# Optimization experiments

Measured on AMD Instinct MI355X. Metric: run time of the kernel, lower is better.

Reference implementation:

```python
import jax, jax.numpy as jnp
import numpy as np

N_HEADS = 16
CHUNK = 128  # chunk size for blocked causal linear attention


def _phi(x):
    # feature map: elu(x) + 1 (strictly positive)
    return jax.nn.elu(x) + 1.0


def setup_inputs() -> dict:
    key = jax.random.key(0)
    ks = jax.random.split(key, 5)
    d = 1024
    scale = (2.0 / (d + d)) ** 0.5  # xavier_uniform-like std
    W = lambda k: jax.random.normal(k, (d, d), jnp.float32) * scale
    return {
        "x": jax.random.normal(ks[0], (4, 4096, d), jnp.float32),
        "Wq": W(ks[1]), "bq": jnp.zeros((d,), jnp.float32),
        "Wk": W(ks[2]), "bk": jnp.zeros((d,), jnp.float32),
        "Wv": W(ks[3]), "bv": jnp.zeros((d,), jnp.float32),
        "Wo": W(ks[4]), "bo": jnp.zeros((d,), jnp.float32),
    }


def reference(x, Wq, bq, Wk, bk, Wv, bv, Wo, bo):
    b, s, dm = x.shape
    h = N_HEADS
    d = dm // h

    def proj(W, bias):
        # (b, s, dm) -> (b*h, s, d)
        y = x @ W.T + bias
        return y.reshape(b, s, h, d).transpose(0, 2, 1, 3).reshape(b * h, s, d)

    q = _phi(proj(Wq, bq))
    k = _phi(proj(Wk, bk))
    v = proj(Wv, bv)

    C = CHUNK
    n = s // C
    # (b*h, s, d) -> (n_chunks, b*h, C, d) for scan over chunks
    to_chunks = lambda t: t.reshape(b * h, n, C, d).transpose(1, 0, 2, 3)
    qc, kc, vc = to_chunks(q), to_chunks(k), to_chunks(v)
    mask = jnp.tril(jnp.ones((C, C), bool))  # causal within chunk

    def step(carry, inp):
        S, z = carry  # S: (bh, d, d) running sum of k v^T; z: (bh, d) running sum of k
        qi, ki, vi = inp  # each (bh, C, d)
        scores = jnp.einsum('bqd,bkd->bqk', qi, ki)
        scores = jnp.where(mask, scores, jnp.zeros((), scores.dtype))
        num = jnp.einsum('bqk,bkd->bqd', scores, vi) + jnp.einsum('bqd,bde->bqe', qi, S)
        kcum = jnp.cumsum(ki, axis=1) + z[:, None, :]
        den = jnp.sum(qi * kcum, axis=-1, keepdims=True)
        out = num / den
        S2 = S + jnp.einsum('bkd,bke->bde', ki, vi)
        z2 = z + ki.sum(axis=1)
        return (S2, z2), out

    init = (jnp.zeros((b * h, d, d), x.dtype), jnp.zeros((b * h, d), x.dtype))
    _, outs = jax.lax.scan(step, init, (qc, kc, vc))  # outs: (n, bh, C, d)
    out = outs.transpose(1, 0, 2, 3).reshape(b, h, s, d).transpose(0, 2, 1, 3).reshape(b, s, dm)
    return out @ Wo.T + bo
```

## Files before the change

kernel.cpp:

```cpp
#include <hip/hip_runtime.h>
#include <hip/hip_bf16.h>

typedef __attribute__((ext_vector_type(8))) short bf16x8;
typedef __attribute__((ext_vector_type(4))) short bf16x4;
typedef __attribute__((ext_vector_type(4))) float floatx4;
typedef unsigned short u16;
typedef unsigned int u32;

#define DM 1024
#define SEQ 4096
#define NH 16
#define HD 64
#define CHUNK 128

__device__ __forceinline__ float bf2f(u16 x) {
    u32 u = ((u32)x) << 16;
    return __builtin_bit_cast(float, u);
}
__device__ __forceinline__ u16 f2bf(float f) {
    u32 u = __builtin_bit_cast(u32, f);
    u32 r = u + 0x7FFF + ((u >> 16) & 1);
    return (u16)(r >> 16);
}
__device__ __forceinline__ bf16x8 cvt8(const float* p) {
    floatx4 a = *(const floatx4*)p;
    floatx4 b = *(const floatx4*)(p + 4);
    bf16x8 r;
    r[0] = (short)f2bf(a[0]); r[1] = (short)f2bf(a[1]);
    r[2] = (short)f2bf(a[2]); r[3] = (short)f2bf(a[3]);
    r[4] = (short)f2bf(b[0]); r[5] = (short)f2bf(b[1]);
    r[6] = (short)f2bf(b[2]); r[7] = (short)f2bf(b[3]);
    return r;
}
__device__ __forceinline__ void async_copy16(const u16* gsrc, u16* ldst) {
    __builtin_amdgcn_global_load_lds(
        (const __attribute__((address_space(1))) void*)gsrc,
        (__attribute__((address_space(3))) void*)ldst, 16, 0, 0);
}

__global__ void cvt_w_k(const float* __restrict__ Wq, const float* __restrict__ Wk,
                        const float* __restrict__ Wv, const float* __restrict__ Wo,
                        u16* __restrict__ Wqkv, u16* __restrict__ Wob)
{
    int g = blockIdx.x * 256 + threadIdx.x;
    int w = g >> 17;
    int off = g & 131071;
    const float* src = (w == 0) ? Wq : (w == 1) ? Wk : (w == 2) ? Wv : Wo;
    u16* dst = (w < 3) ? (Wqkv + ((size_t)w << 20)) : Wob;
    *(bf16x8*)&dst[(size_t)off * 8] = cvt8(src + (size_t)off * 8);
}

__global__ void cvt_x_k(const float* __restrict__ xs, u16* __restrict__ xb)
{
    size_t g = (size_t)blockIdx.x * 256 + threadIdx.x;
    *(bf16x8*)&xb[g * 8] = cvt8(xs + g * 8);
}

__global__ __launch_bounds__(256, 2) void qkv_gemm_k(
    const u16* __restrict__ xb, const u16* __restrict__ Wqkv,
    const float* __restrict__ bq, const float* __restrict__ bk,
    const float* __restrict__ bv,
    u16* __restrict__ Qh, u16* __restrict__ Kh, u16* __restrict__ Vh)
{
    __shared__ __align__(16) u16 aSh[128 * 64];
    __shared__ __align__(16) u16 bSh[128 * 64];
    int t = threadIdx.x, lane = t & 63, w = t >> 6;
    int q = lane >> 4, ln = lane & 15;
    int wm = (w & 1) * 64, wn = (w >> 1) * 64;
    int n0 = blockIdx.x * 128, m0 = blockIdx.y * 128;
    int wgr = t & 192;
    floatx4 acc[4][4] = {};

    for (int k0 = 0; k0 < DM; k0 += 64) {
#pragma unroll
        for (int i = 0; i < 4; ++i) {
            int gi = i * 256 + t;
            int r = gi >> 3;
            int c = (gi & 7) ^ (r & 7);
            async_copy16(xb + (size_t)(m0 + r) * DM + k0 + c * 8,
                         aSh + (size_t)(i * 256 + wgr) * 8);
            async_copy16(Wqkv + (size_t)(n0 + r) * DM + k0 + c * 8,
                         bSh + (size_t)(i * 256 + wgr) * 8);
        }
        __builtin_amdgcn_s_waitcnt(0);
        __syncthreads();
#pragma unroll
        for (int ks = 0; ks < 2; ++ks) {
            int cg = ks * 4 + q;
            bf16x8 af[4], bfv[4];
#pragma unroll
            for (int tm = 0; tm < 4; ++tm) {
                int m = wm + tm * 16 + ln;
                af[tm] = *(const bf16x8*)&aSh[(m * 8 + (cg ^ (m & 7))) * 8];
            }
#pragma unroll
            for (int tn = 0; tn < 4; ++tn) {
                int n = wn + tn * 16 + ln;
                bfv[tn] = *(const bf16x8*)&bSh[(n * 8 + (cg ^ (n & 7))) * 8];
            }
#pragma unroll
            for (int tm = 0; tm < 4; ++tm)
#pragma unroll
                for (int tn = 0; tn < 4; ++tn)
                    acc[tm][tn] = __builtin_amdgcn_mfma_f32_16x16x32_bf16(
                        af[tm], bfv[tn], acc[tm][tn], 0, 0, 0);
        }
        __syncthreads();
    }
#pragma unroll
    for (int tn = 0; tn < 4; ++tn) {
        int gn = n0 + wn + tn * 16 + ln;
        int proj = gn >> 10, col = gn & 1023;
        float bb = ((proj == 0) ? bq : (proj == 1) ? bk : bv)[col];
        u16* plane = (proj == 0) ? Qh : (proj == 1) ? Kh : Vh;
        int head = col >> 6, dl = col & 63;
#pragma unroll
        for (int tm = 0; tm < 4; ++tm) {
            int gmb = m0 + wm + tm * 16 + q * 4;
#pragma unroll
            for (int r = 0; r < 4; ++r) {
                int gm = gmb + r;
                float v = acc[tm][tn][r] + bb;
                if (proj < 2) v = (v > 0.f) ? (v + 1.f) : __expf(v);
                plane[(((size_t)(gm >> 12) * NH + head) * SEQ + (gm & 4095)) * HD + dl]
                    = f2bf(v);
            }
        }
    }
}

__global__ __launch_bounds__(256, 2) void out_gemm_k(
    const u16* __restrict__ Ah, const u16* __restrict__ Wob,
    const float* __restrict__ bo, float* __restrict__ out)
{
    __shared__ __align__(16) u16 aSh[128 * 64];
    __shared__ __align__(16) u16 bSh[128 * 64];
    int t = threadIdx.x, lane = t & 63, w = t >> 6;
    int q = lane >> 4, ln = lane & 15;
    int wm = (w & 1) * 64, wn = (w >> 1) * 64;
    int n0 = blockIdx.x * 128, m0 = blockIdx.y * 128;
    int wgr = t & 192;
    floatx4 acc[4][4] = {};

    for (int k0 = 0; k0 < DM; k0 += 64) {
#pragma unroll
        for (int i = 0; i < 4; ++i) {
            int gi = i * 256 + t;
            int r = gi >> 3;
            int c = (gi & 7) ^ (r & 7);
            int rr = m0 + r;
            async_copy16(Ah + (((size_t)((rr >> 12) * NH + (k0 >> 6))) << 18)
                            + (size_t)((rr & 4095) << 6) + (size_t)(c * 8),
                         aSh + (size_t)(i * 256 + wgr) * 8);
            async_copy16(Wob + (size_t)(n0 + r) * DM + k0 + c * 8,
                         bSh + (size_t)(i * 256 + wgr) * 8);
        }
        __builtin_amdgcn_s_waitcnt(0);
        __syncthreads();
#pragma unroll
        for (int ks = 0; ks < 2; ++ks) {
            int cg = ks * 4 + q;
            bf16x8 af[4], bfv[4];
#pragma unroll
            for (int tm = 0; tm < 4; ++tm) {
                int m = wm + tm * 16 + ln;
                af[tm] = *(const bf16x8*)&aSh[(m * 8 + (cg ^ (m & 7))) * 8];
            }
#pragma unroll
            for (int tn = 0; tn < 4; ++tn) {
                int n = wn + tn * 16 + ln;
                bfv[tn] = *(const bf16x8*)&bSh[(n * 8 + (cg ^ (n & 7))) * 8];
            }
#pragma unroll
            for (int tm = 0; tm < 4; ++tm)
#pragma unroll
                for (int tn = 0; tn < 4; ++tn)
                    acc[tm][tn] = __builtin_amdgcn_mfma_f32_16x16x32_bf16(
                        af[tm], bfv[tn], acc[tm][tn], 0, 0, 0);
        }
        __syncthreads();
    }
#pragma unroll
    for (int tn = 0; tn < 4; ++tn) {
        int gn = n0 + wn + tn * 16 + ln;
        float bb = bo[gn];
#pragma unroll
        for (int tm = 0; tm < 4; ++tm) {
            int gmb = m0 + wm + tm * 16 + q * 4;
#pragma unroll
            for (int r = 0; r < 4; ++r)
                out[(size_t)(gmb + r) * DM + gn] = acc[tm][tn][r] + bb;
        }
    }
}

__global__ __launch_bounds__(256, 1) void chunk_stats_k(
    const u16* __restrict__ Kh, const u16* __restrict__ Vh,
    u16* __restrict__ Sc, float* __restrict__ Zc)
{
    __shared__ __align__(16) u16 kSh[128 * 64];
    __shared__ __align__(16) u16 vSh[128 * 64];
    __shared__ float zpart[4][64];
    int t = threadIdx.x;
    int bhc = blockIdx.x;
    const u16* Kb = Kh + ((size_t)(bhc >> 5) * SEQ + (size_t)(bhc & 31) * CHUNK) * HD;
    const u16* Vb = Vh + ((size_t)(bhc >> 5) * SEQ + (size_t)(bhc & 31) * CHUNK) * HD;
#pragma unroll
    for (int i = 0; i < 4; ++i) {
        int g = i * 256 + t;
        *(bf16x8*)&kSh[g * 8] = *(const bf16x8*)&Kb[(size_t)g * 8];
        *(bf16x8*)&vSh[g * 8] = *(const bf16x8*)&Vb[(size_t)g * 8];
    }
    __syncthreads();
    int tD = t & 15, tE = t >> 4;
    float acc[4][4] = {};
#pragma unroll 8
    for (int r = 0; r < 128; ++r) {
        bf16x4 vq = *(const bf16x4*)&vSh[r * 64 + tE * 4];
        bf16x4 kq = *(const bf16x4*)&kSh[r * 64 + tD * 4];
        float vf[4], kf[4];
#pragma unroll
        for (int i = 0; i < 4; ++i) { vf[i] = bf2f((u16)vq[i]); kf[i] = bf2f((u16)kq[i]); }
#pragma unroll
        for (int a = 0; a < 4; ++a)
#pragma unroll
            for (int b = 0; b < 4; ++b) acc[a][b] += vf[a] * kf[b];
    }
    u16* So = Sc + (size_t)bhc * HD * HD;
#pragma unroll
    for (int a = 0; a < 4; ++a) {
        bf16x4 sv;
#pragma unroll
        for (int b = 0; b < 4; ++b) sv[b] = (short)f2bf(acc[a][b]);
        *(bf16x4*)&So[(tE * 4 + a) * HD + tD * 4] = sv;
    }
    {
        int dz = t & 63, qz = t >> 6;
        float z = 0.f;
#pragma unroll
        for (int r = 0; r < 32; ++r) z += bf2f(kSh[(qz * 32 + r) * 64 + dz]);
        zpart[qz][dz] = z;
    }
    __syncthreads();
    if (t < 64)
        Zc[(size_t)bhc * HD + t] =
            zpart[0][t] + zpart[1][t] + zpart[2][t] + zpart[3][t];
}

__global__ void prefix_k(u16* __restrict__ Sc, float* __restrict__ Zc)
{
    int bh = blockIdx.x, y = blockIdx.y, t = threadIdx.x;
    if (y < 32) {
        size_t base = (size_t)bh * 32 * 4096 + y * 128 + t;
        u16 vals[32];
#pragma unroll
        for (int c = 0; c < 32; ++c) vals[c] = Sc[base + (size_t)c * 4096];
        float run = 0.f;
#pragma unroll
        for (int c = 0; c < 32; ++c) {
            float cur = bf2f(vals[c]);
            Sc[base + (size_t)c * 4096] = f2bf(run);
            run += cur;
        }
    } else if (t < 64) {
        size_t base = (size_t)bh * 32 * 64 + t;
        float zv[32];
#pragma unroll
        for (int c = 0; c < 32; ++c) zv[c] = Zc[base + (size_t)c * 64];
        float run = 0.f;
#pragma unroll
        for (int c = 0; c < 32; ++c) {
            Zc[base + (size_t)c * 64] = run;
            run += zv[c];
        }
    }
}

__global__ __launch_bounds__(256, 1) void attn_out_k(
    const u16* Qh, const u16* __restrict__ Kh,
    const u16* __restrict__ Vh, const u16* __restrict__ Sp,
    const float* __restrict__ Zp, u16* Qw)
{
    __shared__ __align__(16) u16 vtSh[64 * 136];
    __shared__ __align__(16) u16 pSh[128 * 136];
    __shared__ float psum[128];
    __shared__ float qzs[128];
    int t = threadIdx.x, lane = t & 63, w = t >> 6;
    int q = lane >> 4, ln = lane & 15;
    int bhc = blockIdx.x, bh = bhc >> 5, ch = bhc & 31;
    const u16* Qb = Qh + ((size_t)bh * SEQ + (size_t)ch * CHUNK) * HD;
    const u16* Kb = Kh + ((size_t)bh * SEQ + (size_t)ch * CHUNK) * HD;
    const u16* Vb = Vh + ((size_t)bh * SEQ + (size_t)ch * CHUNK) * HD;
    const u16* Spb = Sp + (size_t)bhc * HD * HD;
    const float* Zpb = Zp + (size_t)bhc * HD;

#pragma unroll
    for (int i = 0; i < 4; ++i) {
        int g = i * 256 + t;
        int k = g >> 3, e0 = (g & 7) * 8;
        bf16x8 vv = *(const bf16x8*)&Vb[(size_t)k * HD + e0];
#pragma unroll
        for (int j = 0; j < 8; ++j) vtSh[(e0 + j) * 136 + k] = (u16)vv[j];
    }

    int wm = (w & 1) * 64, wn = (w >> 1) * 64;
    bf16x8 afr[2][4];
#pragma unroll
    for (int ks = 0; ks < 2; ++ks)
#pragma unroll
        for (int tm = 0; tm < 4; ++tm) {
            int m = wm + tm * 16 + ln;
            afr[ks][tm] = *(const bf16x8*)&Qb[(size_t)m * HD + ks * 32 + q * 8];
        }
    floatx4 acc[4][4] = {};
#pragma unroll
    for (int ks = 0; ks < 2; ++ks) {
        bf16x8 bfr[4];
#pragma unroll
        for (int tn = 0; tn < 4; ++tn) {
            int n = wn + tn * 16 + ln;
            bfr[tn] = *(const bf16x8*)&Kb[(size_t)n * HD + ks * 32 + q * 8];
        }
#pragma unroll
        for (int tm = 0; tm < 4; ++tm)
#pragma unroll
            for (int tn = 0; tn < 4; ++tn)
                acc[tm][tn] = __builtin_amdgcn_mfma_f32_16x16x32_bf16(
                    afr[ks][tm], bfr[tn], acc[tm][tn], 0, 0, 0);
    }
#pragma unroll
    for (int tm = 0; tm < 4; ++tm) {
        int rb = wm + tm * 16 + q * 4;
#pragma unroll
        for (int tn = 0; tn < 4; ++tn) {
            int cc = wn + tn * 16 + ln;
#pragma unroll
            for (int r = 0; r < 4; ++r) {
                float v = (cc <= rb + r) ? acc[tm][tn][r] : 0.f;
                pSh[(rb + r) * 136 + cc] = f2bf(v);
            }
        }
    }
    __syncthreads();
    if (t < 128) {
        const u16* prow = &pSh[t * 136];
        float s = 0.f;
#pragma unroll
        for (int i = 0; i < 16; ++i) {
            bf16x8 pv = *(const bf16x8*)&prow[i * 8];
#pragma unroll
            for (int j = 0; j < 8; ++j) s += bf2f((u16)pv[j]);
        }
        psum[t] = s;
    } else {
        int row = t - 128;
        float s = 0.f;
#pragma unroll
        for (int i = 0; i < 8; ++i) {
            bf16x8 qv = *(const bf16x8*)&Qb[(size_t)row * HD + i * 8];
#pragma unroll
            for (int j = 0; j < 8; ++j) s += bf2f((u16)qv[j]) * Zpb[i * 8 + j];
        }
        qzs[row] = s;
    }
    __syncthreads();

    int wn2 = (w >> 1) * 32;
    floatx4 acc2[4][2] = {};
#pragma unroll
    for (int ks = 0; ks < 4; ++ks) {
        bf16x8 ap[4], bv[2];
#pragma unroll
        for (int tm = 0; tm < 4; ++tm) {
            int m = wm + tm * 16 + ln;
            ap[tm] = *(const bf16x8*)&pSh[m * 136 + ks * 32 + q * 8];
        }
#pragma unroll
        for (int tn = 0; tn < 2; ++tn) {
            int n = wn2 + tn * 16 + ln;
            bv[tn] = *(const bf16x8*)&vtSh[n * 136 + ks * 32 + q * 8];
        }
#pragma unroll
        for (int tm = 0; tm < 4; ++tm)
#pragma unroll
            for (int tn = 0; tn < 2; ++tn)
                acc2[tm][tn] = __builtin_amdgcn_mfma_f32_16x16x32_bf16(
                    ap[tm], bv[tn], acc2[tm][tn], 0, 0, 0);
    }
#pragma unroll
    for (int ks = 0; ks < 2; ++ks) {
        bf16x8 bs[2];
#pragma unroll
        for (int tn = 0; tn < 2; ++tn) {
            int n = wn2 + tn * 16 + ln;
            bs[tn] = *(const bf16x8*)&Spb[(size_t)n * HD + ks * 32 + q * 8];
        }
#pragma unroll
        for (int tm = 0; tm < 4; ++tm)
#pragma unroll
            for (int tn = 0; tn < 2; ++tn)
                acc2[tm][tn] = __builtin_amdgcn_mfma_f32_16x16x32_bf16(
                    afr[ks][tm], bs[tn], acc2[tm][tn], 0, 0, 0);
    }
    __syncthreads();
#pragma unroll
    for (int tm = 0; tm < 4; ++tm) {
        int rb = wm + tm * 16 + q * 4;
#pragma unroll
        for (int r = 0; r < 4; ++r) {
            int mrow = rb + r;
            float inv = 1.0f / fmaxf(psum[mrow] + qzs[mrow], 1e-20f);
#pragma unroll
            for (int tn = 0; tn < 2; ++tn) {
                int e = wn2 + tn * 16 + ln;
                pSh[mrow * 72 + e] = f2bf(acc2[tm][tn][r] * inv);
            }
        }
    }
    __syncthreads();
    size_t obase = ((size_t)bh * SEQ + (size_t)ch * CHUNK) * HD;
#pragma unroll
    for (int j = 0; j < 4; ++j) {
        int ci = j * 256 + t;
        *(bf16x8*)&Qw[obase + (size_t)ci * 8] =
            *(const bf16x8*)&pSh[(ci >> 3) * 72 + (ci & 7) * 8];
    }
}

extern "C" void kernel_launch(void* const* d_in, const int* in_sizes, int n_in,
                              void* d_out, int out_size, void* d_ws, size_t ws_size,
                              hipStream_t stream) {
    const float* x  = (const float*)d_in[0];
    const float* Wq = (const float*)d_in[1];
    const float* bq = (const float*)d_in[2];
    const float* Wk = (const float*)d_in[3];
    const float* bk = (const float*)d_in[4];
    const float* Wv = (const float*)d_in[5];
    const float* bv = (const float*)d_in[6];
    const float* Wo = (const float*)d_in[7];
    const float* bo = (const float*)d_in[8];
    float* out = (float*)d_out;

    const size_t PLANE = (size_t)NH * SEQ * HD;
    const size_t FIXED = (3 * (size_t)DM * DM + (size_t)DM * DM) * 2;
    const size_t PER_BATCH = 4 * PLANE * 2 + (size_t)NH * 32 * 4096 * 2
                           + (size_t)NH * 32 * HD * 4;
    if (ws_size < FIXED + PER_BATCH) return;
    int nb = (ws_size >= FIXED + 4 * PER_BATCH) ? 4
           : (ws_size >= FIXED + 2 * PER_BATCH) ? 2 : 1;

    char* p0 = (char*)d_ws;
    u16* Wqkv = (u16*)p0;                       p0 += 3 * (size_t)DM * DM * 2;
    u16* Wob  = (u16*)p0;                       p0 += (size_t)DM * DM * 2;

    cvt_w_k<<<dim3(2048), dim3(256), 0, stream>>>(Wq, Wk, Wv, Wo, Wqkv, Wob);

    for (int b0 = 0; b0 < 4; b0 += nb) {
        char* p = p0;
        u16* xb = (u16*)p;  p += (size_t)nb * PLANE * 2;
        u16* Qh = (u16*)p;  p += (size_t)nb * PLANE * 2;
        u16* Kh = (u16*)p;  p += (size_t)nb * PLANE * 2;
        u16* Vh = (u16*)p;  p += (size_t)nb * PLANE * 2;
        u16* Sc = (u16*)p;  p += (size_t)nb * NH * 32 * 4096 * 2;
        float* Zc = (float*)p;
        const float* xs = x + (size_t)b0 * SEQ * DM;

        cvt_x_k<<<dim3(nb * 2048), dim3(256), 0, stream>>>(xs, xb);
        qkv_gemm_k<<<dim3(24, nb * 32), dim3(256), 0, stream>>>(
            xb, Wqkv, bq, bk, bv, Qh, Kh, Vh);
        chunk_stats_k<<<dim3(nb * 512), dim3(256), 0, stream>>>(Kh, Vh, Sc, Zc);
        prefix_k<<<dim3(nb * 16, 33), dim3(128), 0, stream>>>(Sc, Zc);
        attn_out_k<<<dim3(nb * 512), dim3(256), 0, stream>>>(Qh, Kh, Vh, Sc, Zc, Qh);
        out_gemm_k<<<dim3(8, nb * 32), dim3(256), 0, stream>>>(
            Qh, Wob, bo, out + (size_t)b0 * SEQ * DM);
    }
}
```

Baseline: 381.4 us.

## Rewrite projection GEMMs as 256x256 double-buffered pipelined kernels with swizzled tiles

```diff
diff --git a/kernel.cpp b/kernel.cpp
--- a/kernel.cpp
+++ b/kernel.cpp
@@ -56,71 +56,138 @@
     *(bf16x8*)&xb[g * 8] = cvt8(xs + g * 8);
 }
 
-__global__ __launch_bounds__(256, 2) void qkv_gemm_k(
+template<int CS>
+__device__ __forceinline__ void stage_half(const u16* src, int ld, u16* ldsM,
+                                           int h, int t) {
+#pragma unroll
+    for (int j = 0; j < 2; ++j) {
+        int r  = j * 64 + (t >> 3);
+        int c  = (t & 7) ^ (r & 7);
+        int gr = ((r / CS) * 2 + h) * CS + (r % CS);
+        int wr = j * 64 + ((t & 448) >> 3);
+        int gw = ((wr / CS) * 2 + h) * CS + (wr % CS);
+        async_copy16(src + (size_t)gr * ld + (size_t)c * 8,
+                     ldsM + (size_t)gw * 64);
+    }
+}
+
+__device__ __forceinline__ void ld_a_quad(const u16* aB, int mbase, int ln, int q,
+                                          bf16x8 (&af)[4][2]) {
+#pragma unroll
+    for (int fm = 0; fm < 4; ++fm)
+#pragma unroll
+        for (int ks = 0; ks < 2; ++ks) {
+            int m = mbase + fm * 16 + ln, cg = ks * 4 + q;
+            af[fm][ks] = *(const bf16x8*)&aB[(m * 8 + (cg ^ (m & 7))) * 8];
+        }
+}
+__device__ __forceinline__ void ld_b_pair(const u16* bB, int nbase, int ln, int q,
+                                          bf16x8 (&bf)[2][2]) {
+#pragma unroll
+    for (int fn = 0; fn < 2; ++fn)
+#pragma unroll
+        for (int ks = 0; ks < 2; ++ks) {
+            int n = nbase + fn * 16 + ln, cg = ks * 4 + q;
+            bf[fn][ks] = *(const bf16x8*)&bB[(n * 8 + (cg ^ (n & 7))) * 8];
+        }
+}
+__device__ __forceinline__ void mfma16(const bf16x8 (&af)[4][2],
+                                       const bf16x8 (&bf)[2][2],
+                                       floatx4 (&acc)[8][4], int hm, int gn) {
+#pragma unroll
+    for (int ks = 0; ks < 2; ++ks)
+#pragma unroll
+        for (int fm = 0; fm < 4; ++fm)
+#pragma unroll
+            for (int fn = 0; fn < 2; ++fn)
+                acc[hm * 4 + fm][gn * 2 + fn] =
+                    __builtin_amdgcn_mfma_f32_16x16x32_bf16(
+                        af[fm][ks], bf[fn][ks], acc[hm * 4 + fm][gn * 2 + fn],
+                        0, 0, 0);
+}
+
+#define PH_MID() do { __builtin_amdgcn_sched_barrier(0);                      \
+    __builtin_amdgcn_s_barrier();                                             \
+    asm volatile("s_waitcnt lgkmcnt(0)" ::: "memory");                        \
+    __builtin_amdgcn_sched_barrier(0);                                        \
+    __builtin_amdgcn_s_setprio(1); } while (0)
+#define PH_END() do { __builtin_amdgcn_s_setprio(0);                          \
+    __builtin_amdgcn_sched_barrier(0);                                        \
+    __builtin_amdgcn_s_barrier(); } while (0)
+
+__global__ __launch_bounds__(512, 2) void qkv_gemm_k(
     const u16* __restrict__ xb, const u16* __restrict__ Wqkv,
     const float* __restrict__ bq, const float* __restrict__ bk,
     const float* __restrict__ bv,
     u16* __restrict__ Qh, u16* __restrict__ Kh, u16* __restrict__ Vh)
 {
-    __shared__ __align__(16) u16 aSh[128 * 64];
-    __shared__ __align__(16) u16 bSh[128 * 64];
-    int t = threadIdx.x, lane = t & 63, w = t >> 6;
+    __shared__ __align__(16) u16 lds[2][32768];
+    int t = threadIdx.x, lane = t & 63;
     int q = lane >> 4, ln = lane & 15;
-    int wm = (w & 1) * 64, wn = (w >> 1) * 64;
-    int n0 = blockIdx.x * 128, m0 = blockIdx.y * 128;
-    int wgr = t & 192;
-    floatx4 acc[4][4] = {};
-
-    for (int k0 = 0; k0 < DM; k0 += 64) {
-#pragma unroll
-        for (int i = 0; i < 4; ++i) {
-            int gi = i * 256 + t;
-            int r = gi >> 3;
-            int c = (gi & 7) ^ (r & 7);
-            async_copy16(xb + (size_t)(m0 + r) * DM + k0 + c * 8,
-                         aSh + (size_t)(i * 256 + wgr) * 8);
-            async_copy16(Wqkv + (size_t)(n0 + r) * DM + k0 + c * 8,
-                         bSh + (size_t)(i * 256 + wgr) * 8);
-        }
-        __builtin_amdgcn_s_waitcnt(0);
-        __syncthreads();
-#pragma unroll
-        for (int ks = 0; ks < 2; ++ks) {
-            int cg = ks * 4 + q;
-            bf16x8 af[4], bfv[4];
-#pragma unroll
-            for (int tm = 0; tm < 4; ++tm) {
-                int m = wm + tm * 16 + ln;
-                af[tm] = *(const bf16x8*)&aSh[(m * 8 + (cg ^ (m & 7))) * 8];
-            }
-#pragma unroll
-            for (int tn = 0; tn < 4; ++tn) {
-                int n = wn + tn * 16 + ln;
-                bfv[tn] = *(const bf16x8*)&bSh[(n * 8 + (cg ^ (n & 7))) * 8];
-            }
-#pragma unroll
-            for (int tm = 0; tm < 4; ++tm)
-#pragma unroll
-                for (int tn = 0; tn < 4; ++tn)
-                    acc[tm][tn] = __builtin_amdgcn_mfma_f32_16x16x32_bf16(
-                        af[tm], bfv[tn], acc[tm][tn], 0, 0, 0);
-        }
-        __syncthreads();
-    }
-#pragma unroll
-    for (int tn = 0; tn < 4; ++tn) {
-        int gn = n0 + wn + tn * 16 + ln;
+    int wid = t >> 6;
+    int wmb = (wid >> 2) * 128, wnb = (wid & 3) * 64;
+    int nwg = gridDim.x;
+    int b0i = blockIdx.x;
+    int swz = (b0i & 7) * (nwg >> 3) + (b0i >> 3);
+    int m0 = (swz / 12) * 256, n0 = (swz % 12) * 256;
+
+    const u16* Abase = xb + (size_t)m0 * DM;
+    const u16* Bbase = Wqkv + (size_t)n0 * DM;
+    floatx4 acc[8][4] = {};
+
+    stage_half<64>(Abase + 0,  DM, &lds[0][0],     0, t);
+    stage_half<32>(Bbase + 0,  DM, &lds[0][16384], 1, t);
+    stage_half<64>(Abase + 0,  DM, &lds[0][0],     1, t);
+    stage_half<32>(Bbase + 0,  DM, &lds[0][16384], 0, t);
+    stage_half<64>(Abase + 64, DM, &lds[1][0],     0, t);
+    stage_half<32>(Bbase + 64, DM, &lds[1][16384], 1, t);
+    asm volatile("s_waitcnt vmcnt(4)" ::: "memory");
+    __builtin_amdgcn_sched_barrier(0);
+    __builtin_amdgcn_s_barrier();
+
+#pragma unroll 2
+    for (int tt = 0; tt < 16; ++tt) {
+        const u16* aB = &lds[tt & 1][0];
+        const u16* bB = &lds[tt & 1][16384];
+        u16* aN = &lds[(tt + 1) & 1][0];
+        u16* bN = &lds[(tt + 1) & 1][16384];
+        u16* aC = &lds[tt & 1][0];
+        u16* bC = &lds[tt & 1][16384];
+        bf16x8 af[4][2], bf0[2][2], bf1[2][2];
+        ld_a_quad(aB, wmb, ln, q, af);
+        ld_b_pair(bB, wnb, ln, q, bf0);
+        if (tt < 15) stage_half<64>(Abase + (tt + 1) * 64, DM, aN, 1, t);
+        PH_MID(); mfma16(af, bf0, acc, 0, 0); PH_END();
+        ld_b_pair(bB, wnb + 32, ln, q, bf1);
+        if (tt < 15) stage_half<32>(Bbase + (tt + 1) * 64, DM, bN, 0, t);
+        PH_MID(); mfma16(af, bf1, acc, 0, 1); PH_END();
+        ld_a_quad(aB, wmb + 64, ln, q, af);
+        if (tt < 14) stage_half<64>(Abase + (tt + 2) * 64, DM, aC, 0, t);
+        PH_MID(); mfma16(af, bf1, acc, 1, 1); PH_END();
+        ld_b_pair(bB, wnb, ln, q, bf0);
+        if (tt < 14) stage_half<32>(Bbase + (tt + 2) * 64, DM, bC, 1, t);
+        PH_MID(); mfma16(af, bf0, acc, 1, 0);
+        __builtin_amdgcn_s_setprio(0);
+        if (tt < 14)       asm volatile("s_waitcnt vmcnt(4)" ::: "memory");
+        else if (tt == 14) asm volatile("s_waitcnt vmcnt(0)" ::: "memory");
+        __builtin_amdgcn_sched_barrier(0);
+        __builtin_amdgcn_s_barrier();
+    }
+
+#pragma unroll
+    for (int fn = 0; fn < 4; ++fn) {
+        int gn = n0 + wnb + fn * 16 + ln;
         int proj = gn >> 10, col = gn & 1023;
         float bb = ((proj == 0) ? bq : (proj == 1) ? bk : bv)[col];
         u16* plane = (proj == 0) ? Qh : (proj == 1) ? Kh : Vh;
         int head = col >> 6, dl = col & 63;
 #pragma unroll
-        for (int tm = 0; tm < 4; ++tm) {
-            int gmb = m0 + wm + tm * 16 + q * 4;
+        for (int fm = 0; fm < 8; ++fm) {
+            int gmb = m0 + wmb + fm * 16 + q * 4;
 #pragma unroll
             for (int r = 0; r < 4; ++r) {
                 int gm = gmb + r;
-                float v = acc[tm][tn][r] + bb;
+                float v = acc[fm][fn][r] + bb;
                 if (proj < 2) v = (v > 0.f) ? (v + 1.f) : __expf(v);
                 plane[(((size_t)(gm >> 12) * NH + head) * SEQ + (gm & 4095)) * HD + dl]
                     = f2bf(v);
@@ -129,67 +196,76 @@
     }
 }
 
-__global__ __launch_bounds__(256, 2) void out_gemm_k(
+__global__ __launch_bounds__(512, 2) void out_gemm_k(
     const u16* __restrict__ Ah, const u16* __restrict__ Wob,
     const float* __restrict__ bo, float* __restrict__ out)
 {
-    __shared__ __align__(16) u16 aSh[128 * 64];
-    __shared__ __align__(16) u16 bSh[128 * 64];
-    int t = threadIdx.x, lane = t & 63, w = t >> 6;
+    __shared__ __align__(16) u16 lds[2][32768];
+    int t = threadIdx.x, lane = t & 63;
     int q = lane >> 4, ln = lane & 15;
-    int wm = (w & 1) * 64, wn = (w >> 1) * 64;
-    int n0 = blockIdx.x * 128, m0 = blockIdx.y * 128;
-    int wgr = t & 192;
-    floatx4 acc[4][4] = {};
-
-    for (int k0 = 0; k0 < DM; k0 += 64) {
-#pragma unroll
-        for (int i = 0; i < 4; ++i) {
-            int gi = i * 256 + t;
-            int r = gi >> 3;
-            int c = (gi & 7) ^ (r & 7);
-            int rr = m0 + r;
-            async_copy16(Ah + (((size_t)((rr >> 12) * NH + (k0 >> 6))) << 18)
-                            + (size_t)((rr & 4095) << 6) + (size_t)(c * 8),
-                         aSh + (size_t)(i * 256 + wgr) * 8);
-            async_copy16(Wob + (size_t)(n0 + r) * DM + k0 + c * 8,
-                         bSh + (size_t)(i * 256 + wgr) * 8);
-        }
-        __builtin_amdgcn_s_waitcnt(0);
-        __syncthreads();
-#pragma unroll
-        for (int ks = 0; ks < 2; ++ks) {
-            int cg = ks * 4 + q;
-            bf16x8 af[4], bfv[4];
-#pragma unroll
-            for (int tm = 0; tm < 4; ++tm) {
-                int m = wm + tm * 16 + ln;
-                af[tm] = *(const bf16x8*)&aSh[(m * 8 + (cg ^ (m & 7))) * 8];
-            }
-#pragma unroll
-            for (int tn = 0; tn < 4; ++tn) {
-                int n = wn + tn * 16 + ln;
-                bfv[tn] = *(const bf16x8*)&bSh[(n * 8 + (cg ^ (n & 7))) * 8];
-            }
-#pragma unroll
-            for (int tm = 0; tm < 4; ++tm)
-#pragma unroll
-                for (int tn = 0; tn < 4; ++tn)
-                    acc[tm][tn] = __builtin_amdgcn_mfma_f32_16x16x32_bf16(
-                        af[tm], bfv[tn], acc[tm][tn], 0, 0, 0);
-        }
-        __syncthreads();
-    }
-#pragma unroll
-    for (int tn = 0; tn < 4; ++tn) {
-        int gn = n0 + wn + tn * 16 + ln;
+    int wid = t >> 6;
+    int wmb = (wid >> 2) * 128, wnb = (wid & 3) * 64;
+    int nwg = gridDim.x;
+    int b0i = blockIdx.x;
+    int swz = (b0i & 7) * (nwg >> 3) + (b0i >> 3);
+    int m0 = (swz / 4) * 256, n0 = (swz % 4) * 256;
+
+    const u16* Bbase = Wob + (size_t)n0 * DM;
+    size_t aBlk = (size_t)(m0 >> 12) * NH;
+    size_t aRow = (size_t)(m0 & 4095) * 64;
+    #define ASRC(tt) (Ah + (aBlk + (tt)) * 262144 + aRow)
+    floatx4 acc[8][4] = {};
+
+    stage_half<64>(ASRC(0), 64, &lds[0][0],     0, t);
+    stage_half<32>(Bbase + 0, DM, &lds[0][16384], 1, t);
+    stage_half<64>(ASRC(0), 64, &lds[0][0],     1, t);
+    stage_half<32>(Bbase + 0, DM, &lds[0][16384], 0, t);
+    stage_half<64>(ASRC(1), 64, &lds[1][0],     0, t);
+    stage_half<32>(Bbase + 64, DM, &lds[1][16384], 1, t);
+    asm volatile("s_waitcnt vmcnt(4)" ::: "memory");
+    __builtin_amdgcn_sched_barrier(0);
+    __builtin_amdgcn_s_barrier();
+
+#pragma unroll 2
+    for (int tt = 0; tt < 16; ++tt) {
+        const u16* aB = &lds[tt & 1][0];
+        const u16* bB = &lds[tt & 1][16384];
+        u16* aN = &lds[(tt + 1) & 1][0];
+        u16* bN = &lds[(tt + 1) & 1][16384];
+        u16* aC = &lds[tt & 1][0];
+        u16* bC = &lds[tt & 1][16384];
+        bf16x8 af[4][2], bf0[2][2], bf1[2][2];
+        ld_a_quad(aB, wmb, ln, q, af);
+        ld_b_pair(bB, wnb, ln, q, bf0);
+        if (tt < 15) stage_half<64>(ASRC(tt + 1), 64, aN, 1, t);
+        PH_MID(); mfma16(af, bf0, acc, 0, 0); PH_END();
+        ld_b_pair(bB, wnb + 32, ln, q, bf1);
+        if (tt < 15) stage_half<32>(Bbase + (tt + 1) * 64, DM, bN, 0, t);
+        PH_MID(); mfma16(af, bf1, acc, 0, 1); PH_END();
+        ld_a_quad(aB, wmb + 64, ln, q, af);
+        if (tt < 14) stage_half<64>(ASRC(tt + 2), 64, aC, 0, t);
+        PH_MID(); mfma16(af, bf1, acc, 1, 1); PH_END();
+        ld_b_pair(bB, wnb, ln, q, bf0);
+        if (tt < 14) stage_half<32>(Bbase + (tt + 2) * 64, DM, bC, 1, t);
+        PH_MID(); mfma16(af, bf0, acc, 1, 0);
+        __builtin_amdgcn_s_setprio(0);
+        if (tt < 14)       asm volatile("s_waitcnt vmcnt(4)" ::: "memory");
+        else if (tt == 14) asm volatile("s_waitcnt vmcnt(0)" ::: "memory");
+        __builtin_amdgcn_sched_barrier(0);
+        __builtin_amdgcn_s_barrier();
+    }
+    #undef ASRC
+
+#pragma unroll
+    for (int fn = 0; fn < 4; ++fn) {
+        int gn = n0 + wnb + fn * 16 + ln;
         float bb = bo[gn];
 #pragma unroll
-        for (int tm = 0; tm < 4; ++tm) {
-            int gmb = m0 + wm + tm * 16 + q * 4;
+        for (int fm = 0; fm < 8; ++fm) {
+            int gmb = m0 + wmb + fm * 16 + q * 4;
 #pragma unroll
             for (int r = 0; r < 4; ++r)
-                out[(size_t)(gmb + r) * DM + gn] = acc[tm][tn][r] + bb;
+                out[(size_t)(gmb + r) * DM + gn] = acc[fm][fn][r] + bb;
         }
     }
 }
@@ -466,12 +542,12 @@
         const float* xs = x + (size_t)b0 * SEQ * DM;
 
         cvt_x_k<<<dim3(nb * 2048), dim3(256), 0, stream>>>(xs, xb);
-        qkv_gemm_k<<<dim3(24, nb * 32), dim3(256), 0, stream>>>(
+        qkv_gemm_k<<<dim3(12 * nb * 16), dim3(512), 0, stream>>>(
             xb, Wqkv, bq, bk, bv, Qh, Kh, Vh);
         chunk_stats_k<<<dim3(nb * 512), dim3(256), 0, stream>>>(Kh, Vh, Sc, Zc);
         prefix_k<<<dim3(nb * 16, 33), dim3(128), 0, stream>>>(Sc, Zc);
         attn_out_k<<<dim3(nb * 512), dim3(256), 0, stream>>>(Qh, Kh, Vh, Sc, Zc, Qh);
-        out_gemm_k<<<dim3(8, nb * 32), dim3(256), 0, stream>>>(
+        out_gemm_k<<<dim3(4 * nb * 16), dim3(512), 0, stream>>>(
             Qh, Wob, bo, out + (size_t)b0 * SEQ * DM);
     }
 }
```

Result: slower. 404.9 us (+6.2%).

## Stage QKV epilogue through LDS and remap GEMM blocks per XCD

Applied to the files above, without the earlier changes.

```diff
diff --git a/kernel.cpp b/kernel.cpp
--- a/kernel.cpp
+++ b/kernel.cpp
@@ -60,14 +60,20 @@
     const u16* __restrict__ xb, const u16* __restrict__ Wqkv,
     const float* __restrict__ bq, const float* __restrict__ bk,
     const float* __restrict__ bv,
-    u16* __restrict__ Qh, u16* __restrict__ Kh, u16* __restrict__ Vh)
-{
-    __shared__ __align__(16) u16 aSh[128 * 64];
-    __shared__ __align__(16) u16 bSh[128 * 64];
+    u16* __restrict__ Qh, u16* __restrict__ Kh, u16* __restrict__ Vh,
+    int mblocks)
+{
+    __shared__ __align__(16) u16 sh[2][128 * 64];
+    u16* aSh = sh[0];
+    u16* bSh = sh[1];
     int t = threadIdx.x, lane = t & 63, w = t >> 6;
     int q = lane >> 4, ln = lane & 15;
     int wm = (w & 1) * 64, wn = (w >> 1) * 64;
-    int n0 = blockIdx.x * 128, m0 = blockIdx.y * 128;
+    int bid = blockIdx.x;
+    int xcd = bid & 7, local = bid >> 3;
+    int mPerX = mblocks >> 3;
+    int ml = local % mPerX, nn = local / mPerX;
+    int m0 = (xcd * mPerX + ml) * 128, n0 = nn * 128;
     int wgr = t & 192;
     floatx4 acc[4][4] = {};
 
@@ -107,38 +113,58 @@
         }
         __syncthreads();
     }
+    int proj = n0 >> 10, colb = n0 & 1023;
+    const float* bias = (proj == 0) ? bq : (proj == 1) ? bk : bv;
+    u16* plane = (proj == 0) ? Qh : (proj == 1) ? Kh : Vh;
+    u16* cSh = sh[0];
 #pragma unroll
     for (int tn = 0; tn < 4; ++tn) {
-        int gn = n0 + wn + tn * 16 + ln;
-        int proj = gn >> 10, col = gn & 1023;
-        float bb = ((proj == 0) ? bq : (proj == 1) ? bk : bv)[col];
-        u16* plane = (proj == 0) ? Qh : (proj == 1) ? Kh : Vh;
-        int head = col >> 6, dl = col & 63;
+        int lc = wn + tn * 16 + ln;
+        float bb = bias[colb + lc];
+        int gr = lc >> 3, lo = lc & 7;
 #pragma unroll
         for (int tm = 0; tm < 4; ++tm) {
-            int gmb = m0 + wm + tm * 16 + q * 4;
+            int lrb = wm + tm * 16 + q * 4;
 #pragma unroll
             for (int r = 0; r < 4; ++r) {
-                int gm = gmb + r;
+                int lr = lrb + r;
                 float v = acc[tm][tn][r] + bb;
                 if (proj < 2) v = (v > 0.f) ? (v + 1.f) : __expf(v);
-                plane[(((size_t)(gm >> 12) * NH + head) * SEQ + (gm & 4095)) * HD + dl]
-                    = f2bf(v);
-            }
+                cSh[lr * 128 + ((gr & 8) | ((gr ^ lr) & 7)) * 8 + lo] = f2bf(v);
+            }
+        }
+    }
+    __syncthreads();
+    int head0 = colb >> 6;
+    size_t blk = (size_t)(m0 >> 12);
+    int mrow = m0 & 4095;
+#pragma unroll
+    for (int h = 0; h < 2; ++h) {
+        u16* pb = plane + ((blk * NH + head0 + h) * SEQ + mrow) * HD;
+#pragma unroll
+        for (int it = 0; it < 4; ++it) {
+            int gi = it * 256 + t;
+            int s = gi >> 3, g = gi & 7;
+            *(bf16x8*)&pb[(size_t)gi * 8] =
+                *(const bf16x8*)&cSh[s * 128 + ((h * 8) | (g ^ (s & 7))) * 8];
         }
     }
 }
 
 __global__ __launch_bounds__(256, 2) void out_gemm_k(
     const u16* __restrict__ Ah, const u16* __restrict__ Wob,
-    const float* __restrict__ bo, float* __restrict__ out)
+    const float* __restrict__ bo, float* __restrict__ out, int mblocks)
 {
     __shared__ __align__(16) u16 aSh[128 * 64];
     __shared__ __align__(16) u16 bSh[128 * 64];
     int t = threadIdx.x, lane = t & 63, w = t >> 6;
     int q = lane >> 4, ln = lane & 15;
     int wm = (w & 1) * 64, wn = (w >> 1) * 64;
-    int n0 = blockIdx.x * 128, m0 = blockIdx.y * 128;
+    int bid = blockIdx.x;
+    int xcd = bid & 7, local = bid >> 3;
+    int mPerX = mblocks >> 3;
+    int ml = local % mPerX, nn = local / mPerX;
+    int m0 = (xcd * mPerX + ml) * 128, n0 = nn * 128;
     int wgr = t & 192;
     floatx4 acc[4][4] = {};
 
@@ -464,14 +490,15 @@
         u16* Sc = (u16*)p;  p += (size_t)nb * NH * 32 * 4096 * 2;
         float* Zc = (float*)p;
         const float* xs = x + (size_t)b0 * SEQ * DM;
+        int mblocks = nb * 32;
 
         cvt_x_k<<<dim3(nb * 2048), dim3(256), 0, stream>>>(xs, xb);
-        qkv_gemm_k<<<dim3(24, nb * 32), dim3(256), 0, stream>>>(
-            xb, Wqkv, bq, bk, bv, Qh, Kh, Vh);
+        qkv_gemm_k<<<dim3(24 * mblocks), dim3(256), 0, stream>>>(
+            xb, Wqkv, bq, bk, bv, Qh, Kh, Vh, mblocks);
         chunk_stats_k<<<dim3(nb * 512), dim3(256), 0, stream>>>(Kh, Vh, Sc, Zc);
         prefix_k<<<dim3(nb * 16, 33), dim3(128), 0, stream>>>(Sc, Zc);
         attn_out_k<<<dim3(nb * 512), dim3(256), 0, stream>>>(Qh, Kh, Vh, Sc, Zc, Qh);
-        out_gemm_k<<<dim3(8, nb * 32), dim3(256), 0, stream>>>(
-            Qh, Wob, bo, out + (size_t)b0 * SEQ * DM);
-    }
-}
+        out_gemm_k<<<dim3(8 * mblocks), dim3(256), 0, stream>>>(
+            Qh, Wob, bo, out + (size_t)b0 * SEQ * DM, mblocks);
+    }
+}
```

Result: no change. 378.9 us (-0.6%).
